# Performance work log

Measured on AMD Instinct MI355X. Metric: run time of the kernel, lower is better.

Reference implementation:

```python
import jax, jax.numpy as jnp
import numpy as np

NUM_CELLS = 2048
CELL_DIM = 256
N_STATES = 131072


def setup_inputs() -> dict:
    key = jax.random.key(0)
    k1, k2 = jax.random.split(key)
    x = jax.random.normal(k1, (N_STATES, CELL_DIM), dtype=jnp.float32)
    placeCells = jax.random.normal(k2, (NUM_CELLS, CELL_DIM), dtype=jnp.float32)
    return {"x": x, "placeCells": placeCells}


def reference(x, placeCells):
    # states: (N, cellDim); sims: (N, numCells); output: (N,) int argmax
    states = x.reshape(-1, CELL_DIM)
    sims = jnp.matmul(states, placeCells.T)  # (N, numCells) dense similarity
    return jnp.argmax(sims, axis=1)
```

## Files before the change

kernel.cpp:

```cpp
#include <hip/hip_runtime.h>
#include <float.h>
#include <stdint.h>

#define NUM_CELLS 2048
#define CELL_DIM  256
#define N_STATES  131072

typedef _Float16 half8 __attribute__((ext_vector_type(8)));
typedef float    f32x4 __attribute__((ext_vector_type(4)));
typedef float    f32x4v __attribute__((ext_vector_type(4)));

#define M1 0.10f
#define M2 0.0008f
#define CAP1 32768
#define CAP2 4096

#define WS_C1 0
#define WS_C2 4
#define WS_L1 1024
#define WS_L2 (WS_L1 + 4 * CAP1)
#define WS_PH 262144
#define WS_PL (WS_PH + 1048576)
#define WS_NEEDED (WS_PL + 1048576 + 131072)

#define AS1 __attribute__((address_space(1)))
#define AS3 __attribute__((address_space(3)))

__global__ void prep_p(const float* __restrict__ p, _Float16* __restrict__ ph,
                       _Float16* __restrict__ pl, int* __restrict__ c1,
                       int* __restrict__ c2) {
    int d = blockIdx.x * 256 + threadIdx.x;
    if (d == 0) { *c1 = 0; *c2 = 0; }
    int l = d & 63, kf = (d >> 6) & 7, ct = d >> 9;
    int cell = ct * 16 + (l & 15);
    int k0 = kf * 32 + (l >> 4) * 8;
    const float* s = p + cell * 256 + k0;
    float4 a = *(const float4*)s, b = *(const float4*)(s + 4);
    float v[8] = {a.x, a.y, a.z, a.w, b.x, b.y, b.z, b.w};
    half8 h, lo;
#pragma unroll
    for (int j = 0; j < 8; ++j) {
        _Float16 hi = (_Float16)v[j];
        h[j] = hi;
        lo[j] = (_Float16)((v[j] - (float)hi) * 2048.0f);
    }
    *(half8*)(ph + (size_t)d * 8) = h;
    *(half8*)(pl + (size_t)d * 8) = lo;
}

__launch_bounds__(256, 2)
__global__ void pc_gemm1(const float* __restrict__ x, const _Float16* __restrict__ ph,
                         int* __restrict__ out, int* __restrict__ c1,
                         int* __restrict__ l1) {
    __shared__ _Float16 ringmem[32768];
    char* ring = (char*)ringmem;

    const int tid = threadIdx.x;
    const int l = tid & 63;
    const int w = tid >> 6;

    const char* phb = (const char*)ph;

#pragma unroll
    for (int ss = 0; ss < 3; ++ss) {
        const char* src = phb + ss * 16384 + w * 4096 + (size_t)l * 16;
        char* dst = ring + ss * 16384 + w * 4096;
#pragma unroll
        for (int i = 0; i < 4; ++i)
            __builtin_amdgcn_global_load_lds((const AS1 void*)(src + i * 1024),
                                             (AS3 void*)(dst + i * 1024), 16, 0, 0);
    }
    asm volatile("s_waitcnt vmcnt(4)" ::: "memory");

    const int wrow = blockIdx.x * 128 + w * 32;
    half8 A[2][8];
#pragma unroll
    for (int rt = 0; rt < 2; ++rt)
#pragma unroll
        for (int kf = 0; kf < 8; ++kf) {
            const f32x4v* sp = (const f32x4v*)(x +
                (size_t)(wrow + rt * 16 + (l & 15)) * 256 + kf * 32 + (l >> 4) * 8);
            f32x4v a = __builtin_nontemporal_load(sp);
            f32x4v b = __builtin_nontemporal_load(sp + 1);
            half8 h;
            h[0] = (_Float16)a[0]; h[1] = (_Float16)a[1];
            h[2] = (_Float16)a[2]; h[3] = (_Float16)a[3];
            h[4] = (_Float16)b[0]; h[5] = (_Float16)b[1];
            h[6] = (_Float16)b[2]; h[7] = (_Float16)b[3];
            A[rt][kf] = h;
        }

    asm volatile("s_barrier" ::: "memory");

    const int lofs = l * 16;
    half8 Bf0[8], Bf1[8];
#pragma unroll
    for (int k = 0; k < 8; ++k) {
        Bf0[k] = *(const half8*)(ring + k * 1024 + lofs);
        Bf1[k] = *(const half8*)(ring + 8192 + k * 1024 + lofs);
    }

    float t1[8], t2[8];
    int ic[8];
#pragma unroll
    for (int s = 0; s < 8; ++s) { t1[s] = -FLT_MAX; t2[s] = -FLT_MAX; ic[s] = 0; }

    for (int t = 0; t < 64; ++t) {
        {
            int tn = (t + 3) & 63;
            const char* src = phb + (size_t)tn * 16384 + w * 4096 + (size_t)l * 16;
            char* dst = ring + ((t + 3) & 3) * 16384 + w * 4096;
#pragma unroll
            for (int i = 0; i < 4; ++i)
                __builtin_amdgcn_global_load_lds((const AS1 void*)(src + i * 1024),
                                                 (AS3 void*)(dst + i * 1024), 16, 0, 0);
        }

        const char* nbp = ring + ((t + 1) & 3) * 16384 + lofs;

        f32x4 a00 = {}, a10 = {}, a01 = {}, a11 = {};
#pragma unroll
        for (int k = 0; k < 8; ++k) {
            a00 = __builtin_amdgcn_mfma_f32_16x16x32_f16(A[0][k], Bf0[k], a00, 0, 0, 0);
            a10 = __builtin_amdgcn_mfma_f32_16x16x32_f16(A[1][k], Bf0[k], a10, 0, 0, 0);
            Bf0[k] = *(const half8*)(nbp + k * 1024);
            a01 = __builtin_amdgcn_mfma_f32_16x16x32_f16(A[0][k], Bf1[k], a01, 0, 0, 0);
            a11 = __builtin_amdgcn_mfma_f32_16x16x32_f16(A[1][k], Bf1[k], a11, 0, 0, 0);
            Bf1[k] = *(const half8*)(nbp + 8192 + k * 1024);
        }

#define UPD2(V, TR, CODE)                                                  \
        {                                                                  \
            float v = (V);                                                 \
            float nt2 = __builtin_amdgcn_fmed3f(t1[TR], t2[TR], v);        \
            ic[TR] = (v > t1[TR]) ? (CODE) : ic[TR];                       \
            t1[TR] = fmaxf(t1[TR], v);                                     \
            t2[TR] = nt2;                                                  \
        }
#pragma unroll
        for (int reg = 0; reg < 4; ++reg) {
            UPD2(a00[reg], reg,     t * 2)
            UPD2(a01[reg], reg,     t * 2 + 1)
            UPD2(a10[reg], 4 + reg, t * 2)
            UPD2(a11[reg], 4 + reg, t * 2 + 1)
        }
#undef UPD2

        asm volatile("s_waitcnt vmcnt(4)\n\ts_barrier" ::: "memory");
    }

    asm volatile("s_waitcnt vmcnt(0)" ::: "memory");

    int idx[8];
#pragma unroll
    for (int s = 0; s < 8; ++s) idx[s] = ic[s] * 16 + (l & 15);
#pragma unroll
    for (int m = 1; m <= 8; m <<= 1) {
#pragma unroll
        for (int s = 0; s < 8; ++s) {
            float ot1 = __shfl_xor(t1[s], m, 64);
            int   oi  = __shfl_xor(idx[s], m, 64);
            float ot2 = __shfl_xor(t2[s], m, 64);
            float nt2 = fmaxf(fminf(t1[s], ot1), fmaxf(t2[s], ot2));
            if (ot1 > t1[s] || (ot1 == t1[s] && oi < idx[s])) { t1[s] = ot1; idx[s] = oi; }
            t2[s] = nt2;
        }
    }

#pragma unroll
    for (int s = 0; s < 8; ++s) {
        int rt = s >> 2, reg = s & 3;
        int row = wrow + rt * 16 + (l >> 4) * 4 + reg;
        bool vld = (l & 15) == 0;
        if (vld) out[row] = idx[s];
        bool f = vld && (t1[s] - t2[s] < M1);
        unsigned long long msk = __ballot(f);
        int cnt = __popcll(msk);
        if (cnt) {
            int prefix = __popcll(msk & ((1ull << l) - 1ull));
            int bpos = 0;
            if (l == 0) bpos = atomicAdd(c1, cnt);
            bpos = __shfl(bpos, 0, 64);
            if (f) {
                int pos = bpos + prefix;
                if (pos < CAP1) l1[pos] = row;
            }
        }
    }
}

__launch_bounds__(256, 2)
__global__ void pc_rescue2(const float* __restrict__ x, const _Float16* __restrict__ ph,
                           const _Float16* __restrict__ pl,
                           const int* __restrict__ c1, const int* __restrict__ l1,
                           int* __restrict__ out, int* __restrict__ c2,
                           int* __restrict__ l2) {
    const int n0 = *c1;
    const int n = n0 < CAP1 ? n0 : CAP1;
    const int G = (n + 15) >> 4;
    const int tid = threadIdx.x;
    const int l = tid & 63, wc = tid >> 6;

    __shared__ float rT1[64];
    __shared__ int   rI1[64];
    __shared__ float rT2[64];

    for (int g = blockIdx.x; g < G; g += gridDim.x) {
        const int base = g * 16;
        __syncthreads();

        const int rslot = base + (l & 15);
        const int my_row = l1[rslot < n ? rslot : (n - 1)];

        half8 Ah[8], Al[8];
#pragma unroll
        for (int kf = 0; kf < 8; ++kf) {
            const float* s = x + (size_t)my_row * 256 + kf * 32 + (l >> 4) * 8;
            float4 a = *(const float4*)s, b = *(const float4*)(s + 4);
            float v[8] = {a.x, a.y, a.z, a.w, b.x, b.y, b.z, b.w};
#pragma unroll
            for (int j = 0; j < 8; ++j) {
                _Float16 hi = (_Float16)v[j];
                Ah[kf][j] = hi;
                Al[kf][j] = (_Float16)((v[j] - (float)hi) * 2048.0f);
            }
        }

        const _Float16* bh = ph + wc * 4096 + (size_t)l * 8;
        const _Float16* bl = pl + wc * 4096 + (size_t)l * 8;
        half8 BH[4], BL[4];
#pragma unroll
        for (int j = 0; j < 4; ++j) {
            BH[j] = *(const half8*)(bh + j * 512);
            BL[j] = *(const half8*)(bl + j * 512);
        }

        float t1[4], t2[4];
        int ic[4];
#pragma unroll
        for (int s = 0; s < 4; ++s) { t1[s] = -FLT_MAX; t2[s] = -FLT_MAX; ic[s] = 0; }

        for (int t = 0; t < 32; ++t) {
            const _Float16* bth = bh + t * 16384;
            const _Float16* btl = bl + t * 16384;
            f32x4 hh = {}, hl = {}, lh = {};
#pragma unroll
            for (int k = 0; k < 8; ++k) {
                half8 Bh_ = BH[k & 3], Bl_ = BL[k & 3];
                int off = (k < 4) ? (k + 4) * 512 : (16384 + (k - 4) * 512);
                BH[k & 3] = *(const half8*)(bth + off);
                BL[k & 3] = *(const half8*)(btl + off);
                hh = __builtin_amdgcn_mfma_f32_16x16x32_f16(Ah[k], Bh_, hh, 0, 0, 0);
                hl = __builtin_amdgcn_mfma_f32_16x16x32_f16(Ah[k], Bl_, hl, 0, 0, 0);
                lh = __builtin_amdgcn_mfma_f32_16x16x32_f16(Al[k], Bh_, lh, 0, 0, 0);
            }
#pragma unroll
            for (int reg = 0; reg < 4; ++reg) {
                float v = hh[reg] + (hl[reg] + lh[reg]) * (1.0f / 2048.0f);
                float nt2 = __builtin_amdgcn_fmed3f(t1[reg], t2[reg], v);
                ic[reg] = (v > t1[reg]) ? t : ic[reg];
                t1[reg] = fmaxf(t1[reg], v);
                t2[reg] = nt2;
            }
        }

        int idx[4];
#pragma unroll
        for (int s = 0; s < 4; ++s) idx[s] = (ic[s] * 4 + wc) * 16 + (l & 15);
#pragma unroll
        for (int m = 1; m <= 8; m <<= 1) {
#pragma unroll
            for (int s = 0; s < 4; ++s) {
                float ot1 = __shfl_xor(t1[s], m, 64);
                int   oi  = __shfl_xor(idx[s], m, 64);
                float ot2 = __shfl_xor(t2[s], m, 64);
                float nt2 = fmaxf(fminf(t1[s], ot1), fmaxf(t2[s], ot2));
                if (ot1 > t1[s] || (ot1 == t1[s] && oi < idx[s])) { t1[s] = ot1; idx[s] = oi; }
                t2[s] = nt2;
            }
        }

        if ((l & 15) == 0) {
#pragma unroll
            for (int reg = 0; reg < 4; ++reg) {
                int r = (l >> 4) * 4 + reg;
                rT1[r * 4 + wc] = t1[reg];
                rI1[r * 4 + wc] = idx[reg];
                rT2[r * 4 + wc] = t2[reg];
            }
        }
        __syncthreads();
        if (tid < 16) {
            float T1 = -FLT_MAX, T2 = -FLT_MAX; int I1 = 0x7FFFFFFF;
#pragma unroll
            for (int q = 0; q < 4; ++q) {
                float v1 = rT1[tid * 4 + q];
                int   vi = rI1[tid * 4 + q];
                float v2 = rT2[tid * 4 + q];
                float nt2 = fmaxf(fminf(T1, v1), fmaxf(T2, v2));
                if (v1 > T1 || (v1 == T1 && vi < I1)) { T1 = v1; I1 = vi; }
                T2 = nt2;
            }
            int slot = base + tid;
            if (slot < n) {
                int grow = l1[slot];
                out[grow] = I1;
                if (T1 - T2 < M2) {
                    int pos = atomicAdd(c2, 1);
                    if (pos < CAP2) l2[pos] = grow;
                }
            }
        }
    }
}

__global__ void rescue3(const float* __restrict__ x, const float* __restrict__ p,
                        const int* __restrict__ count, const int* __restrict__ list,
                        int* __restrict__ out) {
    __shared__ float xrow[256];
    __shared__ float pch[32][260];
    __shared__ float red2[32][9];
    __shared__ float bvs[32];
    __shared__ int   bis[32];
    const int tid = threadIdx.x;
    const int n0 = *count;
    const int n = n0 < CAP2 ? n0 : CAP2;
    for (int e = blockIdx.x; e < n; e += gridDim.x) {
        const int row = list[e];
        __syncthreads();
        if (tid < 64) {
            float4 v = *(const float4*)(x + (size_t)row * 256 + tid * 4);
            *(float4*)(&xrow[tid * 4]) = v;
        }
        float bv = -FLT_MAX; int bi = 0;
        const int cell = tid & 31, kq = tid >> 5;
        for (int c0 = 0; c0 < NUM_CELLS; c0 += 32) {
            __syncthreads();
#pragma unroll
            for (int i = 0; i < 8; ++i) {
                int f = tid + i * 256;
                int cr = f >> 6, k4 = (f & 63) * 4;
                float4 v = *(const float4*)(p + (size_t)(c0 + cr) * 256 + k4);
                *(float4*)(&pch[cr][k4]) = v;
            }
            __syncthreads();
            float s = 0.f;
#pragma unroll
            for (int j = 0; j < 8; ++j) {
                float4 pv = *(const float4*)(&pch[cell][kq * 32 + j * 4]);
                float4 xv = *(const float4*)(&xrow[kq * 32 + j * 4]);
                s = fmaf(xv.x, pv.x, s); s = fmaf(xv.y, pv.y, s);
                s = fmaf(xv.z, pv.z, s); s = fmaf(xv.w, pv.w, s);
            }
            red2[cell][kq] = s;
            __syncthreads();
            if (tid < 32) {
                float dot = 0.f;
#pragma unroll
                for (int q = 0; q < 8; ++q) dot += red2[tid][q];
                if (dot > bv) { bv = dot; bi = c0 + tid; }
            }
        }
        if (tid < 32) { bvs[tid] = bv; bis[tid] = bi; }
        __syncthreads();
        if (tid == 0) {
            float B = bvs[0]; int BI = bis[0];
#pragma unroll
            for (int t = 1; t < 32; ++t)
                if (bvs[t] > B || (bvs[t] == B && bis[t] < BI)) { B = bvs[t]; BI = bis[t]; }
            out[row] = BI;
        }
    }
}

#define BM 64
#define BN 64
#define BK 32
#define XP 260
#define PP 68
__launch_bounds__(256, 2)
__global__ void placecells_argmax_fp32(const float* __restrict__ x,
                                       const float* __restrict__ pc,
                                       int* __restrict__ out) {
    __shared__ float xs[BM * XP];
    __shared__ float ps[BK * PP];
    const int tid = threadIdx.x;
    const int tx = tid & 15;
    const int ty = tid >> 4;
    const float* xg = x + (size_t)blockIdx.x * (BM * CELL_DIM);
#pragma unroll
    for (int i = 0; i < 16; ++i) {
        int f = tid + i * 256;
        int s = f >> 6, k4 = (f & 63) << 2;
        *(float4*)(&xs[s * XP + k4]) = *(const float4*)(xg + s * CELL_DIM + k4);
    }
    __syncthreads();
    float runv[4]; int runi[4];
#pragma unroll
    for (int si = 0; si < 4; ++si) { runv[si] = -FLT_MAX; runi[si] = 0; }
    for (int jc = 0; jc < NUM_CELLS; jc += BN) {
        float acc[4][4];
#pragma unroll
        for (int si = 0; si < 4; ++si)
#pragma unroll
            for (int cj = 0; cj < 4; ++cj) acc[si][cj] = 0.0f;
        for (int kc = 0; kc < CELL_DIM; kc += BK) {
            __syncthreads();
#pragma unroll
            for (int i = 0; i < 2; ++i) {
                int f = tid + i * 256;
                int c = f >> 3, k4 = (f & 7) << 2;
                float4 v = *(const float4*)(pc + (size_t)(jc + c) * CELL_DIM + kc + k4);
                ps[(k4 + 0) * PP + c] = v.x; ps[(k4 + 1) * PP + c] = v.y;
                ps[(k4 + 2) * PP + c] = v.z; ps[(k4 + 3) * PP + c] = v.w;
            }
            __syncthreads();
#pragma unroll
            for (int kk = 0; kk < BK; kk += 4) {
                float4 xv[4];
#pragma unroll
                for (int si = 0; si < 4; ++si)
                    xv[si] = *(const float4*)(&xs[(ty * 4 + si) * XP + kc + kk]);
#pragma unroll
                for (int kt = 0; kt < 4; ++kt) {
                    float4 pv = *(const float4*)(&ps[(kk + kt) * PP + tx * 4]);
#pragma unroll
                    for (int si = 0; si < 4; ++si) {
                        float xk = (kt == 0) ? xv[si].x : (kt == 1) ? xv[si].y :
                                   (kt == 2) ? xv[si].z : xv[si].w;
                        acc[si][0] = fmaf(xk, pv.x, acc[si][0]);
                        acc[si][1] = fmaf(xk, pv.y, acc[si][1]);
                        acc[si][2] = fmaf(xk, pv.z, acc[si][2]);
                        acc[si][3] = fmaf(xk, pv.w, acc[si][3]);
                    }
                }
            }
        }
#pragma unroll
        for (int si = 0; si < 4; ++si)
#pragma unroll
            for (int cj = 0; cj < 4; ++cj) {
                int idx = jc + tx * 4 + cj;
                if (acc[si][cj] > runv[si]) { runv[si] = acc[si][cj]; runi[si] = idx; }
            }
    }
    __syncthreads();
    float* rv = ps; int* ri = (int*)(ps + 1024);
#pragma unroll
    for (int si = 0; si < 4; ++si) {
        int s = ty * 4 + si;
        rv[s * 16 + tx] = runv[si]; ri[s * 16 + tx] = runi[si];
    }
    __syncthreads();
    if (tid < BM) {
        float bv = rv[tid * 16]; int bi = ri[tid * 16];
#pragma unroll
        for (int t = 1; t < 16; ++t) {
            float v = rv[tid * 16 + t]; int i = ri[tid * 16 + t];
            if (v > bv || (v == bv && i < bi)) { bv = v; bi = i; }
        }
        out[(size_t)blockIdx.x * BM + tid] = bi;
    }
}

extern "C" void kernel_launch(void* const* d_in, const int* in_sizes, int n_in,
                              void* d_out, int out_size, void* d_ws, size_t ws_size,
                              hipStream_t stream) {
    const float* x  = (const float*)d_in[0];
    const float* pc = (const float*)d_in[1];
    int* out = (int*)d_out;

    if (ws_size >= (size_t)WS_NEEDED) {
        char* ws = (char*)d_ws;
        int* c1 = (int*)(ws + WS_C1);
        int* c2 = (int*)(ws + WS_C2);
        int* l1 = (int*)(ws + WS_L1);
        int* l2 = (int*)(ws + WS_L2);
        _Float16* ph = (_Float16*)(ws + WS_PH);
        _Float16* pl = (_Float16*)(ws + WS_PL);
        prep_p<<<256, 256, 0, stream>>>(pc, ph, pl, c1, c2);
        pc_gemm1<<<N_STATES / 128, 256, 0, stream>>>(x, ph, out, c1, l1);
        pc_rescue2<<<256, 256, 0, stream>>>(x, ph, pl, c1, l1, out, c2, l2);
        rescue3<<<64, 256, 0, stream>>>(x, pc, c2, l2, out);
    } else {
        placecells_argmax_fp32<<<N_STATES / BM, 256, 0, stream>>>(x, pc, out);
    }
}
```

Measured before the change: 444.2 us.

## Shrink LDS ring to three stages and halve B fragments for three blocks per CU

Cuts the shared-memory ring from four to three 16KB stages and splits each iteration into two half-tile MFMA passes that share one set of B-fragment registers. Lower LDS and register use lets the kernel request three resident blocks per CU instead of two, to hide latency better. In exchange it has a shallower prefetch depth (two tiles ahead instead of three) and an extra barrier point inside each iteration.

```diff
diff --git a/kernel.cpp b/kernel.cpp
--- a/kernel.cpp
+++ b/kernel.cpp
@@ -48,11 +48,11 @@
     *(half8*)(pl + (size_t)d * 8) = lo;
 }
 
-__launch_bounds__(256, 2)
+__launch_bounds__(256, 3)
 __global__ void pc_gemm1(const float* __restrict__ x, const _Float16* __restrict__ ph,
                          int* __restrict__ out, int* __restrict__ c1,
                          int* __restrict__ l1) {
-    __shared__ _Float16 ringmem[32768];
+    __shared__ _Float16 ringmem[24576];
     char* ring = (char*)ringmem;
 
     const int tid = threadIdx.x;
@@ -62,7 +62,7 @@
     const char* phb = (const char*)ph;
 
 #pragma unroll
-    for (int ss = 0; ss < 3; ++ss) {
+    for (int ss = 0; ss < 2; ++ss) {
         const char* src = phb + ss * 16384 + w * 4096 + (size_t)l * 16;
         char* dst = ring + ss * 16384 + w * 4096;
 #pragma unroll
@@ -70,7 +70,6 @@
             __builtin_amdgcn_global_load_lds((const AS1 void*)(src + i * 1024),
                                              (AS3 void*)(dst + i * 1024), 16, 0, 0);
     }
-    asm volatile("s_waitcnt vmcnt(4)" ::: "memory");
 
     const int wrow = blockIdx.x * 128 + w * 32;
     half8 A[2][8];
@@ -90,64 +89,74 @@
             A[rt][kf] = h;
         }
 
-    asm volatile("s_barrier" ::: "memory");
+    asm volatile("s_waitcnt vmcnt(4)\n\ts_barrier" ::: "memory");
 
     const int lofs = l * 16;
-    half8 Bf0[8], Bf1[8];
-#pragma unroll
-    for (int k = 0; k < 8; ++k) {
-        Bf0[k] = *(const half8*)(ring + k * 1024 + lofs);
-        Bf1[k] = *(const half8*)(ring + 8192 + k * 1024 + lofs);
-    }
+    half8 Bf[8];
+#pragma unroll
+    for (int k = 0; k < 8; ++k)
+        Bf[k] = *(const half8*)(ring + k * 1024 + lofs);
+
+    char* p0 = ring;
+    char* p1 = ring + 16384;
+    char* p2 = ring + 32768;
 
     float t1[8], t2[8];
     int ic[8];
 #pragma unroll
     for (int s = 0; s < 8; ++s) { t1[s] = -FLT_MAX; t2[s] = -FLT_MAX; ic[s] = 0; }
 
+#define UPD2(V, TR, CODE)                                                  \
+    {                                                                      \
+        float v = (V);                                                     \
+        float nt2 = __builtin_amdgcn_fmed3f(t1[TR], t2[TR], v);            \
+        ic[TR] = (v > t1[TR]) ? (CODE) : ic[TR];                           \
+        t1[TR] = fmaxf(t1[TR], v);                                         \
+        t2[TR] = nt2;                                                      \
+    }
+
     for (int t = 0; t < 64; ++t) {
         {
-            int tn = (t + 3) & 63;
+            int tn = (t + 2) & 63;
             const char* src = phb + (size_t)tn * 16384 + w * 4096 + (size_t)l * 16;
-            char* dst = ring + ((t + 3) & 3) * 16384 + w * 4096;
 #pragma unroll
             for (int i = 0; i < 4; ++i)
                 __builtin_amdgcn_global_load_lds((const AS1 void*)(src + i * 1024),
-                                                 (AS3 void*)(dst + i * 1024), 16, 0, 0);
-        }
-
-        const char* nbp = ring + ((t + 1) & 3) * 16384 + lofs;
-
-        f32x4 a00 = {}, a10 = {}, a01 = {}, a11 = {};
+                                                 (AS3 void*)(p2 + w * 4096 + i * 1024),
+                                                 16, 0, 0);
+        }
+
+        f32x4 a00 = {}, a10 = {};
 #pragma unroll
         for (int k = 0; k < 8; ++k) {
-            a00 = __builtin_amdgcn_mfma_f32_16x16x32_f16(A[0][k], Bf0[k], a00, 0, 0, 0);
-            a10 = __builtin_amdgcn_mfma_f32_16x16x32_f16(A[1][k], Bf0[k], a10, 0, 0, 0);
-            Bf0[k] = *(const half8*)(nbp + k * 1024);
-            a01 = __builtin_amdgcn_mfma_f32_16x16x32_f16(A[0][k], Bf1[k], a01, 0, 0, 0);
-            a11 = __builtin_amdgcn_mfma_f32_16x16x32_f16(A[1][k], Bf1[k], a11, 0, 0, 0);
-            Bf1[k] = *(const half8*)(nbp + 8192 + k * 1024);
-        }
-
-#define UPD2(V, TR, CODE)                                                  \
-        {                                                                  \
-            float v = (V);                                                 \
-            float nt2 = __builtin_amdgcn_fmed3f(t1[TR], t2[TR], v);        \
-            ic[TR] = (v > t1[TR]) ? (CODE) : ic[TR];                       \
-            t1[TR] = fmaxf(t1[TR], v);                                     \
-            t2[TR] = nt2;                                                  \
+            a00 = __builtin_amdgcn_mfma_f32_16x16x32_f16(A[0][k], Bf[k], a00, 0, 0, 0);
+            a10 = __builtin_amdgcn_mfma_f32_16x16x32_f16(A[1][k], Bf[k], a10, 0, 0, 0);
+            Bf[k] = *(const half8*)(p0 + 8192 + k * 1024 + lofs);
         }
 #pragma unroll
         for (int reg = 0; reg < 4; ++reg) {
             UPD2(a00[reg], reg,     t * 2)
+            UPD2(a10[reg], 4 + reg, t * 2)
+        }
+
+        asm volatile("s_waitcnt vmcnt(4)\n\ts_barrier" ::: "memory");
+
+        f32x4 a01 = {}, a11 = {};
+#pragma unroll
+        for (int k = 0; k < 8; ++k) {
+            a01 = __builtin_amdgcn_mfma_f32_16x16x32_f16(A[0][k], Bf[k], a01, 0, 0, 0);
+            a11 = __builtin_amdgcn_mfma_f32_16x16x32_f16(A[1][k], Bf[k], a11, 0, 0, 0);
+            Bf[k] = *(const half8*)(p1 + k * 1024 + lofs);
+        }
+#pragma unroll
+        for (int reg = 0; reg < 4; ++reg) {
             UPD2(a01[reg], reg,     t * 2 + 1)
-            UPD2(a10[reg], 4 + reg, t * 2)
             UPD2(a11[reg], 4 + reg, t * 2 + 1)
         }
+
+        char* tp = p0; p0 = p1; p1 = p2; p2 = tp;
+    }
 #undef UPD2
-
-        asm volatile("s_waitcnt vmcnt(4)\n\ts_barrier" ::: "memory");
-    }
 
     asm volatile("s_waitcnt vmcnt(0)" ::: "memory");
 
```

Result: faster. 434.6 us (-2.2%).
